# Optimization experiments

Hardware: AMD Instinct MI355X
Metric: run time of the kernel (lower is better)

## Reference

```python
import jax, jax.numpy as jnp
import numpy as np

N = 100000      # entity nodes
E = 1000000     # edges per relation
D_IN = 256
HID = 128
EPS = 1e-16     # PyG softmax denominator eps
NEG_SLOPE = 0.2 # GATConv default leaky_relu slope


def _gat_conv(x, ei, Ws, Wd, a_s, a_d, b):
    """Single-head GATConv (heads=1, concat=False) with self-loops."""
    n = x.shape[0]
    loop = jnp.arange(n, dtype=ei.dtype)
    src = jnp.concatenate([ei[0], loop])  # [E+N]
    dst = jnp.concatenate([ei[1], loop])
    h_src = x @ Ws                         # [N, HID]
    h_dst = x @ Wd                         # [N, HID]
    a_src = h_src @ a_s                    # [N]
    a_dst = h_dst @ a_d                    # [N]
    e = jax.nn.leaky_relu(a_src[src] + a_dst[dst], NEG_SLOPE)  # [E+N]
    # numerically-stable softmax over incoming edges of each dst node
    m = jax.ops.segment_max(e, dst, num_segments=n)
    ex = jnp.exp(e - m[dst])
    denom = jax.ops.segment_sum(ex, dst, num_segments=n)
    alpha = ex / (denom[dst] + EPS)        # [E+N]
    out = jax.ops.segment_sum(alpha[:, None] * h_src[src], dst, num_segments=n)
    return out + b


def setup_inputs() -> dict:
    key = jax.random.key(0)
    ks = jax.random.split(key, 9)
    s_in = 1.0 / np.sqrt(D_IN)
    s_h = 1.0 / np.sqrt(HID)
    return {
        "x": jax.random.normal(ks[0], (N, D_IN), dtype=jnp.float32),
        "edge_index_r0": jax.random.randint(ks[1], (2, E), 0, N, dtype=jnp.int64)
                         if jax.config.jax_enable_x64 else jax.random.randint(ks[1], (2, E), 0, N).astype(jnp.int32),
        "edge_index_r1": jax.random.randint(ks[2], (2, E), 0, N, dtype=jnp.int64)
                         if jax.config.jax_enable_x64 else jax.random.randint(ks[2], (2, E), 0, N).astype(jnp.int32),
        "W_src": jax.random.normal(ks[3], (2, D_IN, HID), dtype=jnp.float32) * s_in,
        "W_dst": jax.random.normal(ks[4], (2, D_IN, HID), dtype=jnp.float32) * s_in,
        "att_src": jax.random.normal(ks[5], (2, HID), dtype=jnp.float32) * s_h,
        "att_dst": jax.random.normal(ks[6], (2, HID), dtype=jnp.float32) * s_h,
        "bias": jnp.zeros((2, HID), dtype=jnp.float32),
    }


def reference(x, edge_index_r0, edge_index_r1, W_src, W_dst, att_src, att_dst, bias):
    # HeteroConv aggr='sum' over the two entity->entity relations
    out = _gat_conv(x, edge_index_r0, W_src[0], W_dst[0], att_src[0], att_dst[0], bias[0])
    out = out + _gat_conv(x, edge_index_r1, W_src[1], W_dst[1], att_src[1], att_dst[1], bias[1])
    # ELU; dropout p=0.0 is identity
    return jax.nn.elu(out)
```

## Files before the change

### kernel.cpp

```cpp
#include <hip/hip_runtime.h>

typedef __attribute__((ext_vector_type(8))) __bf16 bf16x8;
typedef __attribute__((ext_vector_type(4))) float floatx4;
typedef __attribute__((ext_vector_type(2))) float floatx2;

__device__ __forceinline__ float bf2f(unsigned short u) {
    return __uint_as_float(((unsigned)u) << 16);
}
__device__ __forceinline__ unsigned short f2bf(float f) {
    unsigned u = __float_as_uint(f);
    unsigned r = u + 0x7FFFu + ((u >> 16) & 1u);
    return (unsigned short)(r >> 16);
}

__device__ __forceinline__ void canon8(const void* src, unsigned short* dst,
                                       long long idx, int f) {
    if (f) {
        *(uint4*)&dst[idx] = *(const uint4*)((const unsigned short*)src + idx);
    } else {
        const float* sf = (const float*)src;
        unsigned short v[8];
        for (int j = 0; j < 8; ++j) v[j] = f2bf(sf[idx + j]);
        *(uint4*)&dst[idx] = *(const uint4*)v;
    }
}

__global__ void detect_k(const unsigned short* __restrict__ xs, int* __restrict__ flag) {
    __shared__ int sred[256];
    int tid = threadIdx.x;
    int cnt = 0;
    for (int j = 0; j < 16; ++j) {
        unsigned short u = xs[(tid * 16 + j) * 2];
        int e = (u >> 7) & 0xFF;
        cnt += (e >= 96 && e <= 159) ? 1 : 0;
    }
    sred[tid] = cnt;
    __syncthreads();
    for (int s = 128; s > 0; s >>= 1) {
        if (tid < s) sred[tid] += sred[tid + s];
        __syncthreads();
    }
    if (tid == 0) *flag = (sred[0] > 2048) ? 1 : 0;
}

__global__ void prep_k(const void* __restrict__ Ws, const void* __restrict__ Wd,
                       const void* __restrict__ as, const void* __restrict__ ad,
                       const void* __restrict__ b,
                       unsigned short* __restrict__ Bt, float* __restrict__ vecs,
                       unsigned short* __restrict__ bsb, const int* __restrict__ flag) {
    int blk = blockIdx.x, tid = threadIdx.x;
    int f = *flag;
    if (blk < 256) {
        int i = blk * 256 + tid;
        int r = i >> 15, rem = i & 32767;
        int k = rem >> 7, nn = rem & 127;
        unsigned short w = f ? ((const unsigned short*)Ws)[i]
                             : f2bf(((const float*)Ws)[i]);
        Bt[(size_t)r * 32768 + nn * 256 + k] = w;
    } else if (blk < 258) {
        int r = blk - 256, k = tid;
        float s = 0.f, t = 0.f;
        if (f) {
            const unsigned short* wsrow = (const unsigned short*)Ws + (size_t)r * 32768 + (size_t)k * 128;
            const unsigned short* wdrow = (const unsigned short*)Wd + (size_t)r * 32768 + (size_t)k * 128;
            const unsigned short* asr = (const unsigned short*)as + r * 128;
            const unsigned short* adr = (const unsigned short*)ad + r * 128;
            for (int h = 0; h < 128; ++h) {
                s += bf2f(wsrow[h]) * bf2f(asr[h]);
                t += bf2f(wdrow[h]) * bf2f(adr[h]);
            }
        } else {
            const float* wsrow = (const float*)Ws + (size_t)r * 32768 + (size_t)k * 128;
            const float* wdrow = (const float*)Wd + (size_t)r * 32768 + (size_t)k * 128;
            const float* asr = (const float*)as + r * 128;
            const float* adr = (const float*)ad + r * 128;
            for (int h = 0; h < 128; ++h) {
                s += wsrow[h] * asr[h];
                t += wdrow[h] * adr[h];
            }
        }
        vecs[(r * 2 + 0) * 256 + k] = s;
        vecs[(r * 2 + 1) * 256 + k] = t;
    } else {
        if (tid < 32) canon8(b, bsb, (long long)tid * 8, f);
    }
}

__device__ __forceinline__ void gload_lds16(const void* g, void* l) {
    __builtin_amdgcn_global_load_lds((const __attribute__((address_space(1))) void*)g,
                                     (__attribute__((address_space(3))) void*)l, 16, 0, 0);
}

__global__ __launch_bounds__(256) void mix1_k(
    const int* __restrict__ ei0, const int* __restrict__ ei1,
    int* __restrict__ cntP, int* __restrict__ rank0, int* __restrict__ rank1,
    int E_, int histB, int period,
    const void* __restrict__ xraw, const unsigned short* __restrict__ Btg,
    unsigned short* __restrict__ hout, int gemmB,
    const float* __restrict__ vecs, float* __restrict__ aout, int n, int canB,
    unsigned long long* __restrict__ pair0, unsigned long long* __restrict__ pair1,
    int ps2, int zB, const int* __restrict__ flag) {
    __shared__ float sv[1024];
    __shared__ __align__(16) unsigned short As[128 * 64];
    __shared__ __align__(16) unsigned short Bs[128 * 64];
    int b = blockIdx.x, tid = threadIdx.x;
    int bq = b / period;
    if (b - bq * period == 0) {
        if (bq >= histB) return;
        int rel = bq & 1;
        int t = ((bq >> 1) << 8) + tid;
        if (t >= E_ + n) return;
        const int* ei = rel ? ei1 : ei0;
        int* rank = rel ? rank1 : rank0;
        int d = (t < E_) ? ei[E_ + t] : (t - E_);
        rank[t] = atomicAdd(&cntP[((rel ? n : 0) + d) << 4], 1);
        return;
    }
    int oid = b - bq - 1;
    if (oid < gemmB) {
        int fl = *flag;
        const int r = oid & 1;
        const unsigned short* bt = Btg + (size_t)r * 32768;
        unsigned short* h = hout + (size_t)r * n * 128;
        const int r0 = (oid >> 1) * 128;
        int lane = tid & 63, wave = tid >> 6;
        int wm = wave >> 1, wn = wave & 1;
        floatx4 acc[4][4];
        for (int mt = 0; mt < 4; ++mt)
            for (int nt = 0; nt < 4; ++nt)
                acc[mt][nt] = (floatx4){0.f, 0.f, 0.f, 0.f};
        int srow = lane >> 3, q = lane & 7;
        int m16 = lane & 15, qb = lane >> 4;
        for (int k0 = 0; k0 < 256; k0 += 64) {
            if (fl) {
                const unsigned short* x = (const unsigned short*)xraw;
                for (int i = 0; i < 4; ++i) {
                    int L = wave * 4 + i;
                    int row = L * 8 + srow;
                    int sw = ((q ^ (row & 7)) << 3);
                    int grow = min(r0 + row, n - 1);
                    gload_lds16(x + (size_t)grow * 256 + k0 + sw, &As[L * 512]);
                    gload_lds16(bt + (size_t)row * 256 + k0 + sw, &Bs[L * 512]);
                }
            } else {
                for (int i = 0; i < 4; ++i) {
                    int L = wave * 4 + i;
                    int row = L * 8 + srow;
                    int sw = ((q ^ (row & 7)) << 3);
                    gload_lds16(bt + (size_t)row * 256 + k0 + sw, &Bs[L * 512]);
                }
                for (int s4 = 0; s4 < 4; ++s4) {
                    int slot = tid * 4 + s4;
                    int row = slot >> 3, q2 = slot & 7;
                    int grow = min(r0 + row, n - 1);
                    const float* src = (const float*)xraw + (size_t)grow * 256 + k0 + q2 * 8;
                    unsigned short v[8];
                    for (int j = 0; j < 8; ++j) v[j] = f2bf(src[j]);
                    *(uint4*)&As[row * 64 + ((q2 ^ (row & 7)) << 3)] = *(const uint4*)v;
                }
            }
            __syncthreads();
            for (int s = 0; s < 2; ++s) {
                int qr = qb + s * 4;
                bf16x8 af[4], bfv[4];
                for (int mt = 0; mt < 4; ++mt) {
                    int row = wm * 64 + mt * 16 + m16;
                    af[mt] = *(const bf16x8*)&As[row * 64 + ((qr ^ (row & 7)) << 3)];
                }
                for (int nt = 0; nt < 4; ++nt) {
                    int row = wn * 64 + nt * 16 + m16;
                    bfv[nt] = *(const bf16x8*)&Bs[row * 64 + ((qr ^ (row & 7)) << 3)];
                }
                for (int mt = 0; mt < 4; ++mt)
                    for (int nt = 0; nt < 4; ++nt)
                        acc[mt][nt] = __builtin_amdgcn_mfma_f32_16x16x32_bf16(
                            af[mt], bfv[nt], acc[mt][nt], 0, 0, 0);
            }
            __syncthreads();
        }
        for (int mt = 0; mt < 4; ++mt) {
            int baser = r0 + wm * 64 + mt * 16 + qb * 4;
            for (int nt = 0; nt < 4; ++nt) {
                int c = wn * 64 + nt * 16 + m16;
                for (int i = 0; i < 4; ++i) {
                    int gr = baser + i;
                    if (gr < n) h[(size_t)gr * 128 + c] = f2bf(acc[mt][nt][i]);
                }
            }
        }
        return;
    }
    oid -= gemmB;
    if (oid < canB) {
        for (int j = 0; j < 4; ++j) sv[j * 256 + tid] = vecs[j * 256 + tid];
        __syncthreads();
        int lane = tid & 63, wave = tid >> 6;
        int row = oid * 4 + wave;
        if (row >= n) return;
        float xf[4];
        if (*flag) {
            uint2 u = *(const uint2*)((const unsigned short*)xraw + (size_t)row * 256 + lane * 4);
            xf[0] = bf2f((unsigned short)(u.x & 0xFFFF));
            xf[1] = bf2f((unsigned short)(u.x >> 16));
            xf[2] = bf2f((unsigned short)(u.y & 0xFFFF));
            xf[3] = bf2f((unsigned short)(u.y >> 16));
        } else {
            float4 f = *(const float4*)((const float*)xraw + (size_t)row * 256 + lane * 4);
            xf[0] = f.x; xf[1] = f.y; xf[2] = f.z; xf[3] = f.w;
        }
        float s[4] = {0.f, 0.f, 0.f, 0.f};
        for (int j = 0; j < 4; ++j)
            for (int qq = 0; qq < 4; ++qq)
                s[j] += xf[qq] * sv[j * 256 + lane * 4 + qq];
        for (int j = 0; j < 4; ++j)
            for (int off = 32; off > 0; off >>= 1)
                s[j] += __shfl_down(s[j], off);
        if (lane == 0)
            for (int j = 0; j < 4; ++j) aout[(size_t)j * n + row] = s[j];
        return;
    }
    oid -= canB;
    if (oid < 2 * zB) {
        unsigned long long* dst = (oid < zB) ? pair0 : pair1;
        int z = (oid < zB) ? oid : oid - zB;
        int idx = z * 256 + tid;
        if (idx < ps2) ((uint4*)dst)[idx] = make_uint4(0u, 0u, 0u, 0u);
    }
}

__global__ __launch_bounds__(256) void scan_red_k(const int* __restrict__ cntP,
                                                  int* __restrict__ part,
                                                  int n, int nb) {
    __shared__ int s[256];
    int rel = blockIdx.y;
    int i = blockIdx.x * 256 + threadIdx.x;
    int v = (i < n) ? ((cntP[((rel ? n : 0) + i) << 4] + 7) & ~7) : 0;
    s[threadIdx.x] = v;
    __syncthreads();
    for (int o = 128; o > 0; o >>= 1) {
        if (threadIdx.x < o) s[threadIdx.x] += s[threadIdx.x + o];
        __syncthreads();
    }
    if (threadIdx.x == 0) part[rel * nb + blockIdx.x] = s[0];
}

__global__ __launch_bounds__(1024) void scan_mid_k(int* __restrict__ part, int nb) {
    __shared__ int s[1024];
    int rel = blockIdx.x;
    int t = threadIdx.x;
    s[t] = (t < nb) ? part[rel * nb + t] : 0;
    __syncthreads();
    for (int o = 1; o < 1024; o <<= 1) {
        int v = (t >= o) ? s[t - o] : 0;
        __syncthreads();
        s[t] += v;
        __syncthreads();
    }
    if (t < nb) part[rel * nb + t] = (t == 0) ? 0 : s[t - 1];
}

__global__ __launch_bounds__(256) void scan_off_k(const int* __restrict__ cntP,
                                                  const int* __restrict__ part,
                                                  int* __restrict__ off0,
                                                  int* __restrict__ off1,
                                                  int n, int nb) {
    __shared__ int s[256];
    int rel = blockIdx.y;
    int* off = rel ? off1 : off0;
    int i = blockIdx.x * 256 + threadIdx.x;
    int t = threadIdx.x;
    int v = (i < n) ? ((cntP[((rel ? n : 0) + i) << 4] + 7) & ~7) : 0;
    s[t] = v;
    __syncthreads();
    for (int o = 1; o < 256; o <<= 1) {
        int u = (t >= o) ? s[t - o] : 0;
        __syncthreads();
        s[t] += u;
        __syncthreads();
    }
    if (i < n) off[i] = part[rel * nb + blockIdx.x] + s[t] - v;
}

__global__ void fill2_k(const int* __restrict__ ei0, const int* __restrict__ ei1,
                        const float* __restrict__ avals,
                        const int* __restrict__ off0, const int* __restrict__ off1,
                        const int* __restrict__ rank0, const int* __restrict__ rank1,
                        unsigned long long* __restrict__ pair0,
                        unsigned long long* __restrict__ pair1,
                        int E_, int n) {
    int rel = blockIdx.y;
    const int* ei = rel ? ei1 : ei0;
    const float* as_ = avals + (rel ? 2 * (size_t)n : 0);
    const float* ad_ = avals + (rel ? 3 * (size_t)n : (size_t)n);
    const int* off = rel ? off1 : off0;
    const int* rank = rel ? rank1 : rank0;
    unsigned long long* pair = rel ? pair1 : pair0;
    int t = blockIdx.x * 256 + threadIdx.x;
    if (t >= E_ + n) return;
    int s, d;
    if (t < E_) { s = ei[t]; d = ei[E_ + t]; } else { s = t - E_; d = s; }
    float e = as_[s] + ad_[d];
    e = e > 0.f ? e : 0.2f * e;
    float w = __expf(e);
    int pos = off[d] + rank[t];
    pair[pos] = ((unsigned long long)__float_as_uint(w) << 32) | (unsigned)s;
}

__device__ __forceinline__ void acc8pk(floatx2* a, float w, const uint4& hv) {
    floatx2 wv = {w, w};
    const unsigned u[4] = {hv.x, hv.y, hv.z, hv.w};
#pragma unroll
    for (int k = 0; k < 4; ++k) {
        floatx2 hf;
        hf.x = __uint_as_float(u[k] << 16);
        hf.y = __uint_as_float(u[k] & 0xFFFF0000u);
        asm("v_pk_fma_f32 %0, %1, %2, %0" : "+v"(a[k]) : "v"(wv), "v"(hf));
    }
}

__device__ __forceinline__ void rel_accP(int s0, int nIt, int g, unsigned l4,
                                         const unsigned long long* __restrict__ pair,
                                         const char* __restrict__ h8,
                                         floatx2* __restrict__ a, float& den) {
    int i = s0 + g;
    unsigned long long p0 = pair[i];
    unsigned long long p1 = pair[i + 4];
    for (int it = 0; it < nIt; ++it) {
        i += 8;
        unsigned long long q0 = pair[i];
        unsigned long long q1 = pair[i + 4];
        uint4 h0 = *(const uint4*)(h8 + ((((unsigned)p0) << 8) + l4));
        uint4 h1 = *(const uint4*)(h8 + ((((unsigned)p1) << 8) + l4));
        float w0 = __uint_as_float((unsigned)(p0 >> 32));
        float w1 = __uint_as_float((unsigned)(p1 >> 32));
        den += w0 + w1;
        acc8pk(a, w0, h0);
        acc8pk(a, w1, h1);
        p0 = q0; p1 = q1;
    }
}

__global__ __launch_bounds__(256) void agg_k(
    const int* __restrict__ off0, const int* __restrict__ off1,
    const int* __restrict__ cntP,
    const unsigned long long* __restrict__ pair0,
    const unsigned long long* __restrict__ pair1,
    const char* __restrict__ h0, const char* __restrict__ h1,
    const unsigned short* __restrict__ bias, void* __restrict__ out,
    int n, const int* __restrict__ flag) {
    int wave = threadIdx.x >> 6, lane = threadIdx.x & 63;
    int g = lane >> 4, l = lane & 15;
    unsigned l4 = (unsigned)l << 4;
    int d = blockIdx.x * 4 + wave;
    if (d >= n) return;

    int sA = off0[d], nItA = (cntP[d << 4] + 7) >> 3;
    int sB = off1[d], nItB = (cntP[(n + d) << 4] + 7) >> 3;

    float denA = 0.f, denB = 0.f;
    floatx2 aA[4], aB[4];
#pragma unroll
    for (int k = 0; k < 4; ++k) {
        aA[k] = (floatx2){0.f, 0.f};
        aB[k] = (floatx2){0.f, 0.f};
    }
    rel_accP(sA, nItA, g, l4, pair0, h0, aA, denA);
    rel_accP(sB, nItB, g, l4, pair1, h1, aB, denB);

    denA += __shfl_xor(denA, 16);
    denA += __shfl_xor(denA, 32);
    denB += __shfl_xor(denB, 16);
    denB += __shfl_xor(denB, 32);
    float invA = __builtin_amdgcn_rcpf(denA + 1e-16f);
    float invB = __builtin_amdgcn_rcpf(denB + 1e-16f);
    floatx2 ivA = {invA, invA}, ivB = {invB, invB};
#pragma unroll
    for (int k = 0; k < 4; ++k) {
        asm("v_pk_mul_f32 %0, %0, %1" : "+v"(aA[k]) : "v"(ivA));
        asm("v_pk_fma_f32 %0, %1, %2, %0" : "+v"(aA[k]) : "v"(aB[k]), "v"(ivB));
    }
    float t8[8] = {aA[0].x, aA[0].y, aA[1].x, aA[1].y,
                   aA[2].x, aA[2].y, aA[3].x, aA[3].y};

    uint4 b0 = *(const uint4*)&bias[l * 8];
    uint4 b1 = *(const uint4*)&bias[128 + l * 8];
    const unsigned* b0u = (const unsigned*)&b0;
    const unsigned* b1u = (const unsigned*)&b1;
    float v[8];
#pragma unroll
    for (int j = 0; j < 8; ++j) {
        float s = t8[j];
        s += __shfl_xor(s, 16);
        s += __shfl_xor(s, 32);
        unsigned w0 = b0u[j >> 1], w1 = b1u[j >> 1];
        float bb = bf2f((unsigned short)((j & 1) ? (w0 >> 16) : (w0 & 0xFFFFu)))
                 + bf2f((unsigned short)((j & 1) ? (w1 >> 16) : (w1 & 0xFFFFu)));
        float t = s + bb;
        v[j] = t > 0.f ? t : (__expf(t) - 1.f);
    }
    if (g == 0) {
        if (*flag) {
            unsigned pk[4];
            for (int j = 0; j < 4; ++j)
                pk[j] = ((unsigned)f2bf(v[2 * j + 1]) << 16) | (unsigned)f2bf(v[2 * j]);
            ((uint4*)out)[(size_t)d * 16 + l] = *(const uint4*)pk;
        } else {
            float4 f0 = make_float4(v[0], v[1], v[2], v[3]);
            float4 f1 = make_float4(v[4], v[5], v[6], v[7]);
            ((float4*)out)[(size_t)d * 32 + l * 2] = f0;
            ((float4*)out)[(size_t)d * 32 + l * 2 + 1] = f1;
        }
    }
}

static inline char* carve(char*& p, size_t bytes) {
    char* r = p;
    p += (bytes + 255) & ~(size_t)255;
    return r;
}

extern "C" void kernel_launch(void* const* d_in, const int* in_sizes, int n_in,
                              void* d_out, int out_size, void* d_ws, size_t ws_size,
                              hipStream_t stream) {
    (void)n_in; (void)out_size; (void)ws_size;
    const void* x_raw  = d_in[0];
    const int*  ei0    = (const int*)d_in[1];
    const int*  ei1    = (const int*)d_in[2];
    const void* Ws_raw = d_in[3];
    const void* Wd_raw = d_in[4];
    const void* as_raw = d_in[5];
    const void* ad_raw = d_in[6];
    const void* b_raw  = d_in[7];

    const int n = in_sizes[0] / 256;
    const int e = in_sizes[1] / 2;
    const int tot = e + n;
    const int nb = (n + 255) / 256;
    const int PS = tot + 7 * n + 32;
    const int ps2 = PS / 2;
    const int zB = (ps2 + 255) / 256;

    char* p = (char*)d_ws;
    float* avals = (float*)carve(p, (size_t)4 * n * 4);
    int*   cntP  = (int*)carve(p, (size_t)2 * n * 64);
    int*   off0  = (int*)carve(p, (size_t)n * 4);
    int*   off1  = (int*)carve(p, (size_t)n * 4);
    int*   part  = (int*)carve(p, (size_t)2 * nb * 4);
    int*   rank0 = (int*)carve(p, (size_t)tot * 4);
    int*   rank1 = (int*)carve(p, (size_t)tot * 4);
    unsigned long long* pair0 = (unsigned long long*)carve(p, (size_t)PS * 8);
    unsigned long long* pair1 = (unsigned long long*)carve(p, (size_t)PS * 8);
    float* vecs  = (float*)carve(p, 1024 * 4);
    int*   flag  = (int*)carve(p, 256);
    unsigned short* h0  = (unsigned short*)carve(p, (size_t)2 * n * 128 * 2);
    unsigned short* h1  = h0 + (size_t)n * 128;
    unsigned short* Bt  = (unsigned short*)carve(p, 65536 * 2);
    unsigned short* bsb = (unsigned short*)carve(p, 256 * 2);

    hipMemsetAsync(cntP, 0, (size_t)2 * n * 64, stream);

    detect_k<<<1, 256, 0, stream>>>((const unsigned short*)x_raw, flag);
    prep_k<<<259, 256, 0, stream>>>(Ws_raw, Wd_raw, as_raw, ad_raw, b_raw,
                                    Bt, vecs, bsb, flag);

    int gb = (tot + 255) / 256;
    int histB = gb * 2;
    int gemmB = ((n + 127) / 128) * 2;
    int canB = (n + 3) / 4;
    int otherTotal = gemmB + canB + 2 * zB;
    int period = (otherTotal + histB - 1) / histB + 1;
    int G = histB * period;
    mix1_k<<<G, 256, 0, stream>>>(
        ei0, ei1, cntP, rank0, rank1, e, histB, period,
        x_raw, Bt, h0, gemmB,
        vecs, avals, n, canB,
        pair0, pair1, ps2, zB, flag);

    scan_red_k<<<dim3(nb, 2), 256, 0, stream>>>(cntP, part, n, nb);
    scan_mid_k<<<2, 1024, 0, stream>>>(part, nb);
    scan_off_k<<<dim3(nb, 2), 256, 0, stream>>>(cntP, part, off0, off1, n, nb);

    fill2_k<<<dim3(gb, 2), 256, 0, stream>>>(ei0, ei1, avals, off0, off1,
                                             rank0, rank1, pair0, pair1, e, n);

    agg_k<<<(n + 3) / 4, 256, 0, stream>>>(off0, off1, cntP, pair0, pair1,
                                           (const char*)h0, (const char*)h1,
                                           bsb, d_out, n, flag);
}
```

Before: 503.7 us.

## Move GEMM from histogram kernel into fill kernel and fold prep into detect

Moves the bf16 GEMM blocks out of the histogram/attention-score kernel and interleaves them with the edge-fill work in a new fused kernel that runs after the offset scan. For fp32 inputs, the attention-score pass also writes a bf16 copy of x, so the GEMM can always use direct global-to-LDS loads. Weight transposition moves into mix1, and the attention-vector precompute plus bias conversion fold into the single-block detect kernel. This changes which phases overlap and removes one launch, at the cost of an extra bf16 x buffer and serial work in one block.

```diff
diff --git a/kernel.cpp b/kernel.cpp
--- a/kernel.cpp
+++ b/kernel.cpp
@@ -25,8 +25,15 @@
     }
 }
 
-__global__ void detect_k(const unsigned short* __restrict__ xs, int* __restrict__ flag) {
+__global__ __launch_bounds__(256) void detect2_k(
+    const unsigned short* __restrict__ xs,
+    const void* __restrict__ Ws, const void* __restrict__ Wd,
+    const void* __restrict__ as, const void* __restrict__ ad,
+    const void* __restrict__ b,
+    int* __restrict__ flag, float* __restrict__ vecs,
+    unsigned short* __restrict__ bsb) {
     __shared__ int sred[256];
+    __shared__ int sflag;
     int tid = threadIdx.x;
     int cnt = 0;
     for (int j = 0; j < 16; ++j) {
@@ -40,25 +47,11 @@
         if (tid < s) sred[tid] += sred[tid + s];
         __syncthreads();
     }
-    if (tid == 0) *flag = (sred[0] > 2048) ? 1 : 0;
-}
-
-__global__ void prep_k(const void* __restrict__ Ws, const void* __restrict__ Wd,
-                       const void* __restrict__ as, const void* __restrict__ ad,
-                       const void* __restrict__ b,
-                       unsigned short* __restrict__ Bt, float* __restrict__ vecs,
-                       unsigned short* __restrict__ bsb, const int* __restrict__ flag) {
-    int blk = blockIdx.x, tid = threadIdx.x;
-    int f = *flag;
-    if (blk < 256) {
-        int i = blk * 256 + tid;
-        int r = i >> 15, rem = i & 32767;
-        int k = rem >> 7, nn = rem & 127;
-        unsigned short w = f ? ((const unsigned short*)Ws)[i]
-                             : f2bf(((const float*)Ws)[i]);
-        Bt[(size_t)r * 32768 + nn * 256 + k] = w;
-    } else if (blk < 258) {
-        int r = blk - 256, k = tid;
+    if (tid == 0) { sflag = (sred[0] > 2048) ? 1 : 0; *flag = sflag; }
+    __syncthreads();
+    int f = sflag;
+    int k = tid;
+    for (int r = 0; r < 2; ++r) {
         float s = 0.f, t = 0.f;
         if (f) {
             const unsigned short* wsrow = (const unsigned short*)Ws + (size_t)r * 32768 + (size_t)k * 128;
@@ -81,28 +74,21 @@
         }
         vecs[(r * 2 + 0) * 256 + k] = s;
         vecs[(r * 2 + 1) * 256 + k] = t;
-    } else {
-        if (tid < 32) canon8(b, bsb, (long long)tid * 8, f);
-    }
-}
-
-__device__ __forceinline__ void gload_lds16(const void* g, void* l) {
-    __builtin_amdgcn_global_load_lds((const __attribute__((address_space(1))) void*)g,
-                                     (__attribute__((address_space(3))) void*)l, 16, 0, 0);
+    }
+    if (tid < 32) canon8(b, bsb, (long long)tid * 8, f);
 }
 
 __global__ __launch_bounds__(256) void mix1_k(
     const int* __restrict__ ei0, const int* __restrict__ ei1,
     int* __restrict__ cntP, int* __restrict__ rank0, int* __restrict__ rank1,
     int E_, int histB, int period,
-    const void* __restrict__ xraw, const unsigned short* __restrict__ Btg,
-    unsigned short* __restrict__ hout, int gemmB,
+    const void* __restrict__ xraw, unsigned short* __restrict__ xb,
     const float* __restrict__ vecs, float* __restrict__ aout, int n, int canB,
     unsigned long long* __restrict__ pair0, unsigned long long* __restrict__ pair1,
-    int ps2, int zB, const int* __restrict__ flag) {
+    int ps2, int zB,
+    const void* __restrict__ Ws, unsigned short* __restrict__ Bt,
+    const int* __restrict__ flag) {
     __shared__ float sv[1024];
-    __shared__ __align__(16) unsigned short As[128 * 64];
-    __shared__ __align__(16) unsigned short Bs[128 * 64];
     int b = blockIdx.x, tid = threadIdx.x;
     int bq = b / period;
     if (b - bq * period == 0) {
@@ -117,12 +103,135 @@
         return;
     }
     int oid = b - bq - 1;
-    if (oid < gemmB) {
-        int fl = *flag;
-        const int r = oid & 1;
+    if (oid < canB) {
+        for (int j = 0; j < 4; ++j) sv[j * 256 + tid] = vecs[j * 256 + tid];
+        __syncthreads();
+        int lane = tid & 63, wave = tid >> 6;
+        int row = oid * 4 + wave;
+        if (row >= n) return;
+        float xf[4];
+        if (*flag) {
+            uint2 u = *(const uint2*)((const unsigned short*)xraw + (size_t)row * 256 + lane * 4);
+            xf[0] = bf2f((unsigned short)(u.x & 0xFFFF));
+            xf[1] = bf2f((unsigned short)(u.x >> 16));
+            xf[2] = bf2f((unsigned short)(u.y & 0xFFFF));
+            xf[3] = bf2f((unsigned short)(u.y >> 16));
+        } else {
+            float4 f = *(const float4*)((const float*)xraw + (size_t)row * 256 + lane * 4);
+            xf[0] = f.x; xf[1] = f.y; xf[2] = f.z; xf[3] = f.w;
+            unsigned short v[4] = {f2bf(f.x), f2bf(f.y), f2bf(f.z), f2bf(f.w)};
+            *(uint2*)&xb[(size_t)row * 256 + lane * 4] = *(const uint2*)v;
+        }
+        float s[4] = {0.f, 0.f, 0.f, 0.f};
+        for (int j = 0; j < 4; ++j)
+            for (int q = 0; q < 4; ++q)
+                s[j] += xf[q] * sv[j * 256 + lane * 4 + q];
+        for (int j = 0; j < 4; ++j)
+            for (int off = 32; off > 0; off >>= 1)
+                s[j] += __shfl_down(s[j], off);
+        if (lane == 0)
+            for (int j = 0; j < 4; ++j) aout[(size_t)j * n + row] = s[j];
+        return;
+    }
+    oid -= canB;
+    if (oid < 2 * zB) {
+        unsigned long long* dst = (oid < zB) ? pair0 : pair1;
+        int z = (oid < zB) ? oid : oid - zB;
+        int idx = z * 256 + tid;
+        if (idx < ps2) ((uint4*)dst)[idx] = make_uint4(0u, 0u, 0u, 0u);
+        return;
+    }
+    oid -= 2 * zB;
+    if (oid < 256) {
+        int i = oid * 256 + tid;
+        int f = *flag;
+        int r = i >> 15, rem = i & 32767;
+        int k = rem >> 7, nn = rem & 127;
+        unsigned short w = f ? ((const unsigned short*)Ws)[i]
+                             : f2bf(((const float*)Ws)[i]);
+        Bt[(size_t)r * 32768 + nn * 256 + k] = w;
+    }
+}
+
+__global__ __launch_bounds__(256) void scan_red_k(const int* __restrict__ cntP,
+                                                  int* __restrict__ part,
+                                                  int n, int nb) {
+    __shared__ int s[256];
+    int rel = blockIdx.y;
+    int i = blockIdx.x * 256 + threadIdx.x;
+    int v = (i < n) ? ((cntP[((rel ? n : 0) + i) << 4] + 7) & ~7) : 0;
+    s[threadIdx.x] = v;
+    __syncthreads();
+    for (int o = 128; o > 0; o >>= 1) {
+        if (threadIdx.x < o) s[threadIdx.x] += s[threadIdx.x + o];
+        __syncthreads();
+    }
+    if (threadIdx.x == 0) part[rel * nb + blockIdx.x] = s[0];
+}
+
+__global__ __launch_bounds__(1024) void scan_mid_k(int* __restrict__ part, int nb) {
+    __shared__ int s[1024];
+    int rel = blockIdx.x;
+    int t = threadIdx.x;
+    s[t] = (t < nb) ? part[rel * nb + t] : 0;
+    __syncthreads();
+    for (int o = 1; o < 1024; o <<= 1) {
+        int v = (t >= o) ? s[t - o] : 0;
+        __syncthreads();
+        s[t] += v;
+        __syncthreads();
+    }
+    if (t < nb) part[rel * nb + t] = (t == 0) ? 0 : s[t - 1];
+}
+
+__global__ __launch_bounds__(256) void scan_off_k(const int* __restrict__ cntP,
+                                                  const int* __restrict__ part,
+                                                  int* __restrict__ off0,
+                                                  int* __restrict__ off1,
+                                                  int n, int nb) {
+    __shared__ int s[256];
+    int rel = blockIdx.y;
+    int* off = rel ? off1 : off0;
+    int i = blockIdx.x * 256 + threadIdx.x;
+    int t = threadIdx.x;
+    int v = (i < n) ? ((cntP[((rel ? n : 0) + i) << 4] + 7) & ~7) : 0;
+    s[t] = v;
+    __syncthreads();
+    for (int o = 1; o < 256; o <<= 1) {
+        int u = (t >= o) ? s[t - o] : 0;
+        __syncthreads();
+        s[t] += u;
+        __syncthreads();
+    }
+    if (i < n) off[i] = part[rel * nb + blockIdx.x] + s[t] - v;
+}
+
+__device__ __forceinline__ void gload_lds16(const void* g, void* l) {
+    __builtin_amdgcn_global_load_lds((const __attribute__((address_space(1))) void*)g,
+                                     (__attribute__((address_space(3))) void*)l, 16, 0, 0);
+}
+
+__global__ __launch_bounds__(256) void mix2_k(
+    const void* __restrict__ x_raw, const unsigned short* __restrict__ xb,
+    const unsigned short* __restrict__ Btg,
+    unsigned short* __restrict__ hout, int n, int gemmB, int period,
+    const int* __restrict__ ei0, const int* __restrict__ ei1,
+    const float* __restrict__ avals,
+    const int* __restrict__ off0, const int* __restrict__ off1,
+    const int* __restrict__ rank0, const int* __restrict__ rank1,
+    unsigned long long* __restrict__ pair0, unsigned long long* __restrict__ pair1,
+    int E_, int fillB, const int* __restrict__ flag) {
+    __shared__ __align__(16) unsigned short As[128 * 64];
+    __shared__ __align__(16) unsigned short Bs[128 * 64];
+    int b = blockIdx.x, tid = threadIdx.x;
+    int bq = b / period;
+    if (b - bq * period == 0) {
+        if (bq >= gemmB) return;
+        const unsigned short* x = (*flag) ? (const unsigned short*)x_raw : xb;
+        const int r = bq & 1;
         const unsigned short* bt = Btg + (size_t)r * 32768;
         unsigned short* h = hout + (size_t)r * n * 128;
-        const int r0 = (oid >> 1) * 128;
+        const int r0 = (bq >> 1) * 128;
         int lane = tid & 63, wave = tid >> 6;
         int wm = wave >> 1, wn = wave & 1;
         floatx4 acc[4][4];
@@ -132,32 +241,13 @@
         int srow = lane >> 3, q = lane & 7;
         int m16 = lane & 15, qb = lane >> 4;
         for (int k0 = 0; k0 < 256; k0 += 64) {
-            if (fl) {
-                const unsigned short* x = (const unsigned short*)xraw;
-                for (int i = 0; i < 4; ++i) {
-                    int L = wave * 4 + i;
-                    int row = L * 8 + srow;
-                    int sw = ((q ^ (row & 7)) << 3);
-                    int grow = min(r0 + row, n - 1);
-                    gload_lds16(x + (size_t)grow * 256 + k0 + sw, &As[L * 512]);
-                    gload_lds16(bt + (size_t)row * 256 + k0 + sw, &Bs[L * 512]);
-                }
-            } else {
-                for (int i = 0; i < 4; ++i) {
-                    int L = wave * 4 + i;
-                    int row = L * 8 + srow;
-                    int sw = ((q ^ (row & 7)) << 3);
-                    gload_lds16(bt + (size_t)row * 256 + k0 + sw, &Bs[L * 512]);
-                }
-                for (int s4 = 0; s4 < 4; ++s4) {
-                    int slot = tid * 4 + s4;
-                    int row = slot >> 3, q2 = slot & 7;
-                    int grow = min(r0 + row, n - 1);
-                    const float* src = (const float*)xraw + (size_t)grow * 256 + k0 + q2 * 8;
-                    unsigned short v[8];
-                    for (int j = 0; j < 8; ++j) v[j] = f2bf(src[j]);
-                    *(uint4*)&As[row * 64 + ((q2 ^ (row & 7)) << 3)] = *(const uint4*)v;
-                }
+            for (int i = 0; i < 4; ++i) {
+                int L = wave * 4 + i;
+                int row = L * 8 + srow;
+                int sw = ((q ^ (row & 7)) << 3);
+                int grow = min(r0 + row, n - 1);
+                gload_lds16(x + (size_t)grow * 256 + k0 + sw, &As[L * 512]);
+                gload_lds16(bt + (size_t)row * 256 + k0 + sw, &Bs[L * 512]);
             }
             __syncthreads();
             for (int s = 0; s < 2; ++s) {
@@ -190,113 +280,17 @@
         }
         return;
     }
-    oid -= gemmB;
-    if (oid < canB) {
-        for (int j = 0; j < 4; ++j) sv[j * 256 + tid] = vecs[j * 256 + tid];
-        __syncthreads();
-        int lane = tid & 63, wave = tid >> 6;
-        int row = oid * 4 + wave;
-        if (row >= n) return;
-        float xf[4];
-        if (*flag) {
-            uint2 u = *(const uint2*)((const unsigned short*)xraw + (size_t)row * 256 + lane * 4);
-            xf[0] = bf2f((unsigned short)(u.x & 0xFFFF));
-            xf[1] = bf2f((unsigned short)(u.x >> 16));
-            xf[2] = bf2f((unsigned short)(u.y & 0xFFFF));
-            xf[3] = bf2f((unsigned short)(u.y >> 16));
-        } else {
-            float4 f = *(const float4*)((const float*)xraw + (size_t)row * 256 + lane * 4);
-            xf[0] = f.x; xf[1] = f.y; xf[2] = f.z; xf[3] = f.w;
-        }
-        float s[4] = {0.f, 0.f, 0.f, 0.f};
-        for (int j = 0; j < 4; ++j)
-            for (int qq = 0; qq < 4; ++qq)
-                s[j] += xf[qq] * sv[j * 256 + lane * 4 + qq];
-        for (int j = 0; j < 4; ++j)
-            for (int off = 32; off > 0; off >>= 1)
-                s[j] += __shfl_down(s[j], off);
-        if (lane == 0)
-            for (int j = 0; j < 4; ++j) aout[(size_t)j * n + row] = s[j];
-        return;
-    }
-    oid -= canB;
-    if (oid < 2 * zB) {
-        unsigned long long* dst = (oid < zB) ? pair0 : pair1;
-        int z = (oid < zB) ? oid : oid - zB;
-        int idx = z * 256 + tid;
-        if (idx < ps2) ((uint4*)dst)[idx] = make_uint4(0u, 0u, 0u, 0u);
-    }
-}
-
-__global__ __launch_bounds__(256) void scan_red_k(const int* __restrict__ cntP,
-                                                  int* __restrict__ part,
-                                                  int n, int nb) {
-    __shared__ int s[256];
-    int rel = blockIdx.y;
-    int i = blockIdx.x * 256 + threadIdx.x;
-    int v = (i < n) ? ((cntP[((rel ? n : 0) + i) << 4] + 7) & ~7) : 0;
-    s[threadIdx.x] = v;
-    __syncthreads();
-    for (int o = 128; o > 0; o >>= 1) {
-        if (threadIdx.x < o) s[threadIdx.x] += s[threadIdx.x + o];
-        __syncthreads();
-    }
-    if (threadIdx.x == 0) part[rel * nb + blockIdx.x] = s[0];
-}
-
-__global__ __launch_bounds__(1024) void scan_mid_k(int* __restrict__ part, int nb) {
-    __shared__ int s[1024];
-    int rel = blockIdx.x;
-    int t = threadIdx.x;
-    s[t] = (t < nb) ? part[rel * nb + t] : 0;
-    __syncthreads();
-    for (int o = 1; o < 1024; o <<= 1) {
-        int v = (t >= o) ? s[t - o] : 0;
-        __syncthreads();
-        s[t] += v;
-        __syncthreads();
-    }
-    if (t < nb) part[rel * nb + t] = (t == 0) ? 0 : s[t - 1];
-}
-
-__global__ __launch_bounds__(256) void scan_off_k(const int* __restrict__ cntP,
-                                                  const int* __restrict__ part,
-                                                  int* __restrict__ off0,
-                                                  int* __restrict__ off1,
-                                                  int n, int nb) {
-    __shared__ int s[256];
-    int rel = blockIdx.y;
-    int* off = rel ? off1 : off0;
-    int i = blockIdx.x * 256 + threadIdx.x;
-    int t = threadIdx.x;
-    int v = (i < n) ? ((cntP[((rel ? n : 0) + i) << 4] + 7) & ~7) : 0;
-    s[t] = v;
-    __syncthreads();
-    for (int o = 1; o < 256; o <<= 1) {
-        int u = (t >= o) ? s[t - o] : 0;
-        __syncthreads();
-        s[t] += u;
-        __syncthreads();
-    }
-    if (i < n) off[i] = part[rel * nb + blockIdx.x] + s[t] - v;
-}
-
-__global__ void fill2_k(const int* __restrict__ ei0, const int* __restrict__ ei1,
-                        const float* __restrict__ avals,
-                        const int* __restrict__ off0, const int* __restrict__ off1,
-                        const int* __restrict__ rank0, const int* __restrict__ rank1,
-                        unsigned long long* __restrict__ pair0,
-                        unsigned long long* __restrict__ pair1,
-                        int E_, int n) {
-    int rel = blockIdx.y;
+    int fid = b - bq - 1;
+    if (fid >= fillB) return;
+    int rel = fid & 1;
+    int t = ((fid >> 1) << 8) + tid;
+    if (t >= E_ + n) return;
     const int* ei = rel ? ei1 : ei0;
     const float* as_ = avals + (rel ? 2 * (size_t)n : 0);
     const float* ad_ = avals + (rel ? 3 * (size_t)n : (size_t)n);
     const int* off = rel ? off1 : off0;
     const int* rank = rel ? rank1 : rank0;
     unsigned long long* pair = rel ? pair1 : pair0;
-    int t = blockIdx.x * 256 + threadIdx.x;
-    if (t >= E_ + n) return;
     int s, d;
     if (t < E_) { s = ei[t]; d = ei[E_ + t]; } else { s = t - E_; d = s; }
     float e = as_[s] + ad_[d];
@@ -452,6 +446,7 @@
     unsigned long long* pair1 = (unsigned long long*)carve(p, (size_t)PS * 8);
     float* vecs  = (float*)carve(p, 1024 * 4);
     int*   flag  = (int*)carve(p, 256);
+    unsigned short* xb  = (unsigned short*)carve(p, (size_t)(n + 128) * 256 * 2);
     unsigned short* h0  = (unsigned short*)carve(p, (size_t)2 * n * 128 * 2);
     unsigned short* h1  = h0 + (size_t)n * 128;
     unsigned short* Bt  = (unsigned short*)carve(p, 65536 * 2);
@@ -459,29 +454,32 @@
 
     hipMemsetAsync(cntP, 0, (size_t)2 * n * 64, stream);
 
-    detect_k<<<1, 256, 0, stream>>>((const unsigned short*)x_raw, flag);
-    prep_k<<<259, 256, 0, stream>>>(Ws_raw, Wd_raw, as_raw, ad_raw, b_raw,
-                                    Bt, vecs, bsb, flag);
+    detect2_k<<<1, 256, 0, stream>>>((const unsigned short*)x_raw, Ws_raw, Wd_raw,
+                                     as_raw, ad_raw, b_raw, flag, vecs, bsb);
 
     int gb = (tot + 255) / 256;
     int histB = gb * 2;
-    int gemmB = ((n + 127) / 128) * 2;
     int canB = (n + 3) / 4;
-    int otherTotal = gemmB + canB + 2 * zB;
+    int otherTotal = canB + 2 * zB + 256;
     int period = (otherTotal + histB - 1) / histB + 1;
     int G = histB * period;
     mix1_k<<<G, 256, 0, stream>>>(
         ei0, ei1, cntP, rank0, rank1, e, histB, period,
-        x_raw, Bt, h0, gemmB,
-        vecs, avals, n, canB,
-        pair0, pair1, ps2, zB, flag);
+        x_raw, xb, vecs, avals, n, canB,
+        pair0, pair1, ps2, zB,
+        Ws_raw, Bt, flag);
 
     scan_red_k<<<dim3(nb, 2), 256, 0, stream>>>(cntP, part, n, nb);
     scan_mid_k<<<2, 1024, 0, stream>>>(part, nb);
     scan_off_k<<<dim3(nb, 2), 256, 0, stream>>>(cntP, part, off0, off1, n, nb);
 
-    fill2_k<<<dim3(gb, 2), 256, 0, stream>>>(ei0, ei1, avals, off0, off1,
-                                             rank0, rank1, pair0, pair1, e, n);
+    int gemmB = ((n + 127) / 128) * 2;
+    int fillB = gb * 2;
+    int period2 = (fillB + gemmB - 1) / gemmB + 1;
+    int G2 = gemmB * period2;
+    mix2_k<<<G2, 256, 0, stream>>>(
+        x_raw, xb, Bt, h0, n, gemmB, period2,
+        ei0, ei1, avals, off0, off1, rank0, rank1, pair0, pair1, e, fillB, flag);
 
     agg_k<<<(n + 3) / 4, 256, 0, stream>>>(off0, off1, cntP, pair0, pair1,
                                            (const char*)h0, (const char*)h1,
```

After: 464.7 us. 1.08x faster.
